# Kernel optimization log

Hardware: AMD Instinct MI355X
Metric: run time of the kernel (lower is better)

The kernel has to match this reference:

```python
import jax, jax.numpy as jnp
import numpy as np

B, IN_F, K_INT, OUT_F = 256, 512, 75, 64
INIT = 0.05


def setup_inputs() -> dict:
    key = jax.random.key(0)
    k_x, k_t = jax.random.split(key)
    x = jax.random.normal(k_x, (B, IN_F), dtype=jnp.float32)
    T = jax.random.normal(k_t, (IN_F, K_INT, OUT_F), dtype=jnp.float32) * INIT
    return {"x": x, "T": T}


def reference(x, T):
    # M: [B, K, O] = x @ T flattened over (K, O)
    Bn = x.shape[0]
    M = (x @ T.reshape(T.shape[0], -1)).reshape(Bn, T.shape[1], T.shape[2])
    # pairwise L1 distance over K: [B, B, O]
    # (original materializes [B, B, K, O] broadcasted diff; same math)
    M_diff = M[None, :, :, :] - M[:, None, :, :]
    distance = jnp.abs(M_diff).sum(axis=2)           # [B, B, O]
    exp_distance = jnp.exp(-distance)                # [B, B, O]
    minibatch_features = exp_distance.sum(axis=1) - 1.0  # [B, O]; -1 removes self-distance
    return minibatch_features
```

## Files before the change

### kernel.cpp

```cpp
#include <hip/hip_runtime.h>


typedef __attribute__((ext_vector_type(8))) short bf16x8;
typedef __attribute__((ext_vector_type(4))) float f32x4;
typedef unsigned short ushort_t;
typedef unsigned int uint_t;

__device__ inline ushort_t f2bf(float f) {
  uint_t u = __float_as_uint(f);
  return (ushort_t)((u + 0x7FFFu + ((u >> 16) & 1u)) >> 16);
}

__global__ __launch_bounds__(256) void cvt_x(const float* __restrict__ x,
                                             ushort_t* __restrict__ xb) {
  const int i = blockIdx.x * 256 + threadIdx.x;
  const float4* x4 = reinterpret_cast<const float4*>(x);
  const float4 v0 = x4[i * 2], v1 = x4[i * 2 + 1];
  uint4 o;
  o.x = (uint_t)f2bf(v0.x) | ((uint_t)f2bf(v0.y) << 16);
  o.y = (uint_t)f2bf(v0.z) | ((uint_t)f2bf(v0.w) << 16);
  o.z = (uint_t)f2bf(v1.x) | ((uint_t)f2bf(v1.y) << 16);
  o.w = (uint_t)f2bf(v1.z) | ((uint_t)f2bf(v1.w) << 16);
  *reinterpret_cast<uint4*>(xb + i * 8) = o;
}

__global__ __launch_bounds__(256) void cvt_T(const float* __restrict__ T,
                                             ushort_t* __restrict__ Tb) {
  const int f0 = blockIdx.x << 6;
  const int k = blockIdx.y;
  const int tid = threadIdx.x;
  __shared__ float tile[64][65];

  const float4* T4 = reinterpret_cast<const float4*>(T);
  const int r = tid >> 2;
  const int c = tid & 3;
#pragma unroll
  for (int h = 0; h < 4; ++h) {
    const int q = c + (h << 2);
    const float4 v = T4[(f0 + r) * 1200 + k * 16 + q];
    tile[r][(q << 2) + 0] = v.x;
    tile[r][(q << 2) + 1] = v.y;
    tile[r][(q << 2) + 2] = v.z;
    tile[r][(q << 2) + 3] = v.w;
  }
  __syncthreads();

  const int w = tid >> 2;
  ushort_t us[16];
#pragma unroll
  for (int j = 0; j < 16; ++j) us[j] = f2bf(tile[(c << 4) + j][w]);
  uint4 p0, p1;
  p0.x = (uint_t)us[0] | ((uint_t)us[1] << 16);
  p0.y = (uint_t)us[2] | ((uint_t)us[3] << 16);
  p0.z = (uint_t)us[4] | ((uint_t)us[5] << 16);
  p0.w = (uint_t)us[6] | ((uint_t)us[7] << 16);
  p1.x = (uint_t)us[8] | ((uint_t)us[9] << 16);
  p1.y = (uint_t)us[10] | ((uint_t)us[11] << 16);
  p1.z = (uint_t)us[12] | ((uint_t)us[13] << 16);
  p1.w = (uint_t)us[14] | ((uint_t)us[15] << 16);
  uint4* dst = reinterpret_cast<uint4*>(Tb + ((k << 6) + w) * 512 + f0 + (c << 4));
  dst[0] = p0;
  dst[1] = p1;
}

__global__ __launch_bounds__(256) void md_gemm_mfma(const ushort_t* __restrict__ Tb,
                                                    const ushort_t* __restrict__ xb,
                                                    float* __restrict__ Mt) {
  const int tid = threadIdx.x;
  const int l = tid & 63, w = tid >> 6;
  const int n0 = (blockIdx.x << 6) + ((w >> 1) << 5);
  const int b0 = (blockIdx.y << 6) + ((w & 1) << 5);
  const int lr = l & 15;
  const int ko = (l >> 4) << 3;

  const ushort_t* pa0 = Tb + (n0 + lr) * 512 + ko;
  const ushort_t* pa1 = pa0 + 16 * 512;
  const ushort_t* pb0 = xb + (b0 + lr) * 512 + ko;
  const ushort_t* pb1 = pb0 + 16 * 512;

  f32x4 d00 = {0.f, 0.f, 0.f, 0.f}, d01 = d00, d10 = d00, d11 = d00;

#pragma unroll 4
  for (int kk = 0; kk < 16; ++kk) {
    const int off = kk << 5;
    const bf16x8 a0 = *reinterpret_cast<const bf16x8*>(pa0 + off);
    const bf16x8 a1 = *reinterpret_cast<const bf16x8*>(pa1 + off);
    const bf16x8 f0 = *reinterpret_cast<const bf16x8*>(pb0 + off);
    const bf16x8 f1 = *reinterpret_cast<const bf16x8*>(pb1 + off);
    d00 = __builtin_amdgcn_mfma_f32_16x16x32_bf16(a0, f0, d00, 0, 0, 0);
    d01 = __builtin_amdgcn_mfma_f32_16x16x32_bf16(a0, f1, d01, 0, 0, 0);
    d10 = __builtin_amdgcn_mfma_f32_16x16x32_bf16(a1, f0, d10, 0, 0, 0);
    d11 = __builtin_amdgcn_mfma_f32_16x16x32_bf16(a1, f1, d11, 0, 0, 0);
  }

#pragma unroll
  for (int r = 0; r < 4; ++r) {
    const int row = ((l >> 4) << 2) + r;
    {
      const int n = n0 + row;
      float* base = Mt + (n & 63) * 19200 + (n >> 6) * 256;
      base[b0 + lr] = d00[r];
      base[b0 + 16 + lr] = d01[r];
    }
    {
      const int n = n0 + 16 + row;
      float* base = Mt + (n & 63) * 19200 + (n >> 6) * 256;
      base[b0 + lr] = d10[r];
      base[b0 + 16 + lr] = d11[r];
    }
  }
}

__global__ __launch_bounds__(256) void md_pair(const float* __restrict__ Mt,
                                               float* __restrict__ out) {
  const int o = blockIdx.x;
  const int ibase = blockIdx.y << 5;
  const int tid = threadIdx.x;
  const int io = tid & 15;
  const int jg = tid >> 4;

  __shared__ alignas(16) float Ms[38 * 256];

  float d0[16], d1[16];
#pragma unroll
  for (int q = 0; q < 16; ++q) { d0[q] = 0.0f; d1[q] = 0.0f; }

  const int i0 = ibase + (io << 1);

  for (int kh = 0; kh < 2; ++kh) {
    const int nk = kh ? 37 : 38;
    {
      const float4* src4 = reinterpret_cast<const float4*>(Mt + o * 19200 + kh * (38 * 256));
      float4* dst4 = reinterpret_cast<float4*>(Ms);
      const int n4 = nk << 6;
      for (int idx = tid; idx < n4; idx += 256) dst4[idx] = src4[idx];
    }
    __syncthreads();

    for (int k = 0; k < nk; ++k) {
      const float* row = Ms + (k << 8);
      const float mi0 = row[i0];
      const float mi1 = row[i0 + 1];
      const float4* row4 = reinterpret_cast<const float4*>(row) + (jg << 2);
#pragma unroll
      for (int q = 0; q < 4; ++q) {
        const float4 v = row4[q];
        d0[4 * q + 0] += __builtin_fabsf(v.x - mi0);
        d0[4 * q + 1] += __builtin_fabsf(v.y - mi0);
        d0[4 * q + 2] += __builtin_fabsf(v.z - mi0);
        d0[4 * q + 3] += __builtin_fabsf(v.w - mi0);
        d1[4 * q + 0] += __builtin_fabsf(v.x - mi1);
        d1[4 * q + 1] += __builtin_fabsf(v.y - mi1);
        d1[4 * q + 2] += __builtin_fabsf(v.z - mi1);
        d1[4 * q + 3] += __builtin_fabsf(v.w - mi1);
      }
    }
    __syncthreads();
  }

  float s0 = 0.0f, s1 = 0.0f;
#pragma unroll
  for (int q = 0; q < 16; ++q) {
    s0 += __expf(-d0[q]);
    s1 += __expf(-d1[q]);
  }

  float* red = Ms;
  red[((io << 1) + 0) * 17 + jg] = s0;
  red[((io << 1) + 1) * 17 + jg] = s1;
  __syncthreads();
  if (tid < 32) {
    float s = 0.0f;
#pragma unroll
    for (int g = 0; g < 16; ++g) s += red[tid * 17 + g];
    out[(ibase + tid) * 64 + o] = s - 1.0f;
  }
}

extern "C" void kernel_launch(void* const* d_in, const int* in_sizes, int n_in,
                              void* d_out, int out_size, void* d_ws, size_t ws_size,
                              hipStream_t stream) {
  const float* x = (const float*)d_in[0];
  const float* T = (const float*)d_in[1];
  float* out = (float*)d_out;

  char* ws = (char*)d_ws;
  float* Mt = (float*)ws;
  ushort_t* Tb = (ushort_t*)(ws + 4915200);
  ushort_t* xb = (ushort_t*)(ws + 9830400);

  cvt_x<<<64, 256, 0, stream>>>(x, xb);
  cvt_T<<<dim3(8, 75), 256, 0, stream>>>(T, Tb);
  md_gemm_mfma<<<dim3(75, 4), 256, 0, stream>>>(Tb, xb, Mt);
  md_pair<<<dim3(64, 8), 256, 0, stream>>>(Mt, out);
}
```

Measured before the change: 57.73 us.

## Fuse MFMA GEMM into pairwise L1 kernel, keeping M tile in LDS

Merges the GEMM and pairwise-distance kernels. Each block recomputes M[:, :, o] for all 256 batch rows with MFMA straight into shared memory, which removes the global Mt round trip and one launch. T is re-laid out padded to 80 K-rows per output feature, and the 37.5KB... wait, 80x276 floats (about 88KB) of LDS holds all 75 K rows at once, so the two-phase reload goes away. The cost is that each of the 4 i-blocks per o redoes the same GEMM, and the large LDS footprint with 512 threads limits occupancy.

After: 87.35 us. 1.51x slower.

```diff
diff --git a/kernel.cpp b/kernel.cpp
--- a/kernel.cpp
+++ b/kernel.cpp
@@ -3,40 +3,50 @@
 
 typedef __attribute__((ext_vector_type(8))) short bf16x8;
 typedef __attribute__((ext_vector_type(4))) float f32x4;
-typedef unsigned short ushort_t;
-typedef unsigned int uint_t;
+typedef unsigned short u16;
+typedef unsigned int u32;
 
-__device__ inline ushort_t f2bf(float f) {
-  uint_t u = __float_as_uint(f);
-  return (ushort_t)((u + 0x7FFFu + ((u >> 16) & 1u)) >> 16);
+__device__ inline u16 f2bf(float f) {
+  u32 u = __float_as_uint(f);
+  return (u16)((u + 0x7FFFu + ((u >> 16) & 1u)) >> 16);
 }
 
 __global__ __launch_bounds__(256) void cvt_x(const float* __restrict__ x,
-                                             ushort_t* __restrict__ xb) {
+                                             u16* __restrict__ xb) {
   const int i = blockIdx.x * 256 + threadIdx.x;
   const float4* x4 = reinterpret_cast<const float4*>(x);
   const float4 v0 = x4[i * 2], v1 = x4[i * 2 + 1];
   uint4 o;
-  o.x = (uint_t)f2bf(v0.x) | ((uint_t)f2bf(v0.y) << 16);
-  o.y = (uint_t)f2bf(v0.z) | ((uint_t)f2bf(v0.w) << 16);
-  o.z = (uint_t)f2bf(v1.x) | ((uint_t)f2bf(v1.y) << 16);
-  o.w = (uint_t)f2bf(v1.z) | ((uint_t)f2bf(v1.w) << 16);
+  o.x = (u32)f2bf(v0.x) | ((u32)f2bf(v0.y) << 16);
+  o.y = (u32)f2bf(v0.z) | ((u32)f2bf(v0.w) << 16);
+  o.z = (u32)f2bf(v1.x) | ((u32)f2bf(v1.y) << 16);
+  o.w = (u32)f2bf(v1.z) | ((u32)f2bf(v1.w) << 16);
   *reinterpret_cast<uint4*>(xb + i * 8) = o;
 }
 
 __global__ __launch_bounds__(256) void cvt_T(const float* __restrict__ T,
-                                             ushort_t* __restrict__ Tb) {
+                                             u16* __restrict__ Tb) {
   const int f0 = blockIdx.x << 6;
   const int k = blockIdx.y;
   const int tid = threadIdx.x;
+  const int w = tid >> 2;
+  const int c = tid & 3;
+  u16* dst = Tb + (w * 80 + k) * 512 + f0 + (c << 4);
+
+  if (k >= 75) {
+    const uint4 z = make_uint4(0, 0, 0, 0);
+    reinterpret_cast<uint4*>(dst)[0] = z;
+    reinterpret_cast<uint4*>(dst)[1] = z;
+    return;
+  }
+
   __shared__ float tile[64][65];
-
   const float4* T4 = reinterpret_cast<const float4*>(T);
-  const int r = tid >> 2;
-  const int c = tid & 3;
 #pragma unroll
   for (int h = 0; h < 4; ++h) {
-    const int q = c + (h << 2);
+    const int idx = (h << 8) + tid;
+    const int r = idx >> 4;
+    const int q = idx & 15;
     const float4 v = T4[(f0 + r) * 1200 + k * 16 + q];
     tile[r][(q << 2) + 0] = v.x;
     tile[r][(q << 2) + 1] = v.y;
@@ -45,131 +55,102 @@
   }
   __syncthreads();
 
-  const int w = tid >> 2;
-  ushort_t us[16];
+  u16 us[16];
 #pragma unroll
   for (int j = 0; j < 16; ++j) us[j] = f2bf(tile[(c << 4) + j][w]);
   uint4 p0, p1;
-  p0.x = (uint_t)us[0] | ((uint_t)us[1] << 16);
-  p0.y = (uint_t)us[2] | ((uint_t)us[3] << 16);
-  p0.z = (uint_t)us[4] | ((uint_t)us[5] << 16);
-  p0.w = (uint_t)us[6] | ((uint_t)us[7] << 16);
-  p1.x = (uint_t)us[8] | ((uint_t)us[9] << 16);
-  p1.y = (uint_t)us[10] | ((uint_t)us[11] << 16);
-  p1.z = (uint_t)us[12] | ((uint_t)us[13] << 16);
-  p1.w = (uint_t)us[14] | ((uint_t)us[15] << 16);
-  uint4* dst = reinterpret_cast<uint4*>(Tb + ((k << 6) + w) * 512 + f0 + (c << 4));
-  dst[0] = p0;
-  dst[1] = p1;
+  p0.x = (u32)us[0] | ((u32)us[1] << 16);
+  p0.y = (u32)us[2] | ((u32)us[3] << 16);
+  p0.z = (u32)us[4] | ((u32)us[5] << 16);
+  p0.w = (u32)us[6] | ((u32)us[7] << 16);
+  p1.x = (u32)us[8] | ((u32)us[9] << 16);
+  p1.y = (u32)us[10] | ((u32)us[11] << 16);
+  p1.z = (u32)us[12] | ((u32)us[13] << 16);
+  p1.w = (u32)us[14] | ((u32)us[15] << 16);
+  reinterpret_cast<uint4*>(dst)[0] = p0;
+  reinterpret_cast<uint4*>(dst)[1] = p1;
 }
 
-__global__ __launch_bounds__(256) void md_gemm_mfma(const ushort_t* __restrict__ Tb,
-                                                    const ushort_t* __restrict__ xb,
-                                                    float* __restrict__ Mt) {
+#define MROW 276
+__global__ __launch_bounds__(512, 2) void md_fused(const u16* __restrict__ Tb,
+                                                   const u16* __restrict__ xb,
+                                                   float* __restrict__ out) {
+  const int o = blockIdx.x;
+  const int ibase = blockIdx.y << 6;
   const int tid = threadIdx.x;
-  const int l = tid & 63, w = tid >> 6;
-  const int n0 = (blockIdx.x << 6) + ((w >> 1) << 5);
-  const int b0 = (blockIdx.y << 6) + ((w & 1) << 5);
-  const int lr = l & 15;
-  const int ko = (l >> 4) << 3;
 
-  const ushort_t* pa0 = Tb + (n0 + lr) * 512 + ko;
-  const ushort_t* pa1 = pa0 + 16 * 512;
-  const ushort_t* pb0 = xb + (b0 + lr) * 512 + ko;
-  const ushort_t* pb1 = pb0 + 16 * 512;
+  __shared__ float Ms[80 * MROW];
 
-  f32x4 d00 = {0.f, 0.f, 0.f, 0.f}, d01 = d00, d10 = d00, d11 = d00;
-
+  {
+    const int l = tid & 63, w = tid >> 6;
+    const int b0 = w << 5;
+    const int lr = l & 15;
+    const int ko = (l >> 4) << 3;
+    const u16* A = Tb + o * (80 * 512);
+    const u16* B0 = xb + (b0 + lr) * 512 + ko;
+    const u16* B1 = B0 + 16 * 512;
+#pragma unroll
+    for (int kt = 0; kt < 5; ++kt) {
+      const u16* Ak = A + (kt * 16 + lr) * 512 + ko;
+      f32x4 d0 = {0.f, 0.f, 0.f, 0.f}, d1 = d0;
 #pragma unroll 4
-  for (int kk = 0; kk < 16; ++kk) {
-    const int off = kk << 5;
-    const bf16x8 a0 = *reinterpret_cast<const bf16x8*>(pa0 + off);
-    const bf16x8 a1 = *reinterpret_cast<const bf16x8*>(pa1 + off);
-    const bf16x8 f0 = *reinterpret_cast<const bf16x8*>(pb0 + off);
-    const bf16x8 f1 = *reinterpret_cast<const bf16x8*>(pb1 + off);
-    d00 = __builtin_amdgcn_mfma_f32_16x16x32_bf16(a0, f0, d00, 0, 0, 0);
-    d01 = __builtin_amdgcn_mfma_f32_16x16x32_bf16(a0, f1, d01, 0, 0, 0);
-    d10 = __builtin_amdgcn_mfma_f32_16x16x32_bf16(a1, f0, d10, 0, 0, 0);
-    d11 = __builtin_amdgcn_mfma_f32_16x16x32_bf16(a1, f1, d11, 0, 0, 0);
-  }
-
+      for (int ks = 0; ks < 16; ++ks) {
+        const bf16x8 a  = *reinterpret_cast<const bf16x8*>(Ak + (ks << 5));
+        const bf16x8 f0 = *reinterpret_cast<const bf16x8*>(B0 + (ks << 5));
+        const bf16x8 f1 = *reinterpret_cast<const bf16x8*>(B1 + (ks << 5));
+        d0 = __builtin_amdgcn_mfma_f32_16x16x32_bf16(a, f0, d0, 0, 0, 0);
+        d1 = __builtin_amdgcn_mfma_f32_16x16x32_bf16(a, f1, d1, 0, 0, 0);
+      }
 #pragma unroll
-  for (int r = 0; r < 4; ++r) {
-    const int row = ((l >> 4) << 2) + r;
-    {
-      const int n = n0 + row;
-      float* base = Mt + (n & 63) * 19200 + (n >> 6) * 256;
-      base[b0 + lr] = d00[r];
-      base[b0 + 16 + lr] = d01[r];
-    }
-    {
-      const int n = n0 + 16 + row;
-      float* base = Mt + (n & 63) * 19200 + (n >> 6) * 256;
-      base[b0 + lr] = d10[r];
-      base[b0 + 16 + lr] = d11[r];
+      for (int r = 0; r < 4; ++r) {
+        const int k = kt * 16 + ((l >> 4) << 2) + r;
+        Ms[k * MROW + b0 + lr] = d0[r];
+        Ms[k * MROW + b0 + 16 + lr] = d1[r];
+      }
     }
   }
-}
+  __syncthreads();
 
-__global__ __launch_bounds__(256) void md_pair(const float* __restrict__ Mt,
-                                               float* __restrict__ out) {
-  const int o = blockIdx.x;
-  const int ibase = blockIdx.y << 5;
-  const int tid = threadIdx.x;
-  const int io = tid & 15;
-  const int jg = tid >> 4;
+  const int io = tid & 31;
+  const int jg = tid >> 5;
+  const int iL = ibase + (io << 1);
 
-  __shared__ alignas(16) float Ms[38 * 256];
+  float d0a[16], d1a[16];
+#pragma unroll
+  for (int q = 0; q < 16; ++q) { d0a[q] = 0.0f; d1a[q] = 0.0f; }
 
-  float d0[16], d1[16];
+  for (int k = 0; k < 75; ++k) {
+    const float* row = Ms + k * MROW;
+    const float mi0 = row[iL];
+    const float mi1 = row[iL + 1];
+    const float4* row4 = reinterpret_cast<const float4*>(row) + (jg << 2);
 #pragma unroll
-  for (int q = 0; q < 16; ++q) { d0[q] = 0.0f; d1[q] = 0.0f; }
-
-  const int i0 = ibase + (io << 1);
-
-  for (int kh = 0; kh < 2; ++kh) {
-    const int nk = kh ? 37 : 38;
-    {
-      const float4* src4 = reinterpret_cast<const float4*>(Mt + o * 19200 + kh * (38 * 256));
-      float4* dst4 = reinterpret_cast<float4*>(Ms);
-      const int n4 = nk << 6;
-      for (int idx = tid; idx < n4; idx += 256) dst4[idx] = src4[idx];
+    for (int q = 0; q < 4; ++q) {
+      const float4 v = row4[q];
+      d0a[4 * q + 0] += __builtin_fabsf(v.x - mi0);
+      d0a[4 * q + 1] += __builtin_fabsf(v.y - mi0);
+      d0a[4 * q + 2] += __builtin_fabsf(v.z - mi0);
+      d0a[4 * q + 3] += __builtin_fabsf(v.w - mi0);
+      d1a[4 * q + 0] += __builtin_fabsf(v.x - mi1);
+      d1a[4 * q + 1] += __builtin_fabsf(v.y - mi1);
+      d1a[4 * q + 2] += __builtin_fabsf(v.z - mi1);
+      d1a[4 * q + 3] += __builtin_fabsf(v.w - mi1);
     }
-    __syncthreads();
-
-    for (int k = 0; k < nk; ++k) {
-      const float* row = Ms + (k << 8);
-      const float mi0 = row[i0];
-      const float mi1 = row[i0 + 1];
-      const float4* row4 = reinterpret_cast<const float4*>(row) + (jg << 2);
-#pragma unroll
-      for (int q = 0; q < 4; ++q) {
-        const float4 v = row4[q];
-        d0[4 * q + 0] += __builtin_fabsf(v.x - mi0);
-        d0[4 * q + 1] += __builtin_fabsf(v.y - mi0);
-        d0[4 * q + 2] += __builtin_fabsf(v.z - mi0);
-        d0[4 * q + 3] += __builtin_fabsf(v.w - mi0);
-        d1[4 * q + 0] += __builtin_fabsf(v.x - mi1);
-        d1[4 * q + 1] += __builtin_fabsf(v.y - mi1);
-        d1[4 * q + 2] += __builtin_fabsf(v.z - mi1);
-        d1[4 * q + 3] += __builtin_fabsf(v.w - mi1);
-      }
-    }
-    __syncthreads();
   }
 
   float s0 = 0.0f, s1 = 0.0f;
 #pragma unroll
   for (int q = 0; q < 16; ++q) {
-    s0 += __expf(-d0[q]);
-    s1 += __expf(-d1[q]);
+    s0 += __expf(-d0a[q]);
+    s1 += __expf(-d1a[q]);
   }
 
+  __syncthreads();
   float* red = Ms;
   red[((io << 1) + 0) * 17 + jg] = s0;
   red[((io << 1) + 1) * 17 + jg] = s1;
   __syncthreads();
-  if (tid < 32) {
+  if (tid < 64) {
     float s = 0.0f;
 #pragma unroll
     for (int g = 0; g < 16; ++g) s += red[tid * 17 + g];
@@ -185,12 +166,10 @@
   float* out = (float*)d_out;
 
   char* ws = (char*)d_ws;
-  float* Mt = (float*)ws;
-  ushort_t* Tb = (ushort_t*)(ws + 4915200);
-  ushort_t* xb = (ushort_t*)(ws + 9830400);
+  u16* Tb = (u16*)ws;
+  u16* xb = (u16*)(ws + 5242880);
 
   cvt_x<<<64, 256, 0, stream>>>(x, xb);
-  cvt_T<<<dim3(8, 75), 256, 0, stream>>>(T, Tb);
-  md_gemm_mfma<<<dim3(75, 4), 256, 0, stream>>>(Tb, xb, Mt);
-  md_pair<<<dim3(64, 8), 256, 0, stream>>>(Mt, out);
+  cvt_T<<<dim3(8, 80), 256, 0, stream>>>(T, Tb);
+  md_fused<<<dim3(64, 4), 512, 0, stream>>>(Tb, xb, out);
 }
```

## Exploit distance symmetry with upper-triangular tile pairs and a reduce kernel

Applied to the files above, without the earlier changes.

The pairwise kernel now computes only the upper-triangular 64x64 tile pairs of the batch-by-batch distance matrix for each output feature. Each off-diagonal tile contributes both row sums and column sums to the partial results, and a new reduce kernel adds the partials and subtracts the self term. Each thread now computes a 4x4 register block from float4 loads instead of 2x16. This cuts the abs-diff arithmetic by roughly 40% but adds a kernel launch, extra reductions and more shared memory per block (about 38KB).

Measured after the change: 53.24 us. 1.08x faster.

```diff
diff --git a/kernel.cpp b/kernel.cpp
--- a/kernel.cpp
+++ b/kernel.cpp
@@ -3,29 +3,29 @@
 
 typedef __attribute__((ext_vector_type(8))) short bf16x8;
 typedef __attribute__((ext_vector_type(4))) float f32x4;
-typedef unsigned short ushort_t;
-typedef unsigned int uint_t;
-
-__device__ inline ushort_t f2bf(float f) {
-  uint_t u = __float_as_uint(f);
-  return (ushort_t)((u + 0x7FFFu + ((u >> 16) & 1u)) >> 16);
+typedef unsigned short u16;
+typedef unsigned int u32;
+
+__device__ inline u16 f2bf(float f) {
+  u32 u = __float_as_uint(f);
+  return (u16)((u + 0x7FFFu + ((u >> 16) & 1u)) >> 16);
 }
 
 __global__ __launch_bounds__(256) void cvt_x(const float* __restrict__ x,
-                                             ushort_t* __restrict__ xb) {
+                                             u16* __restrict__ xb) {
   const int i = blockIdx.x * 256 + threadIdx.x;
   const float4* x4 = reinterpret_cast<const float4*>(x);
   const float4 v0 = x4[i * 2], v1 = x4[i * 2 + 1];
   uint4 o;
-  o.x = (uint_t)f2bf(v0.x) | ((uint_t)f2bf(v0.y) << 16);
-  o.y = (uint_t)f2bf(v0.z) | ((uint_t)f2bf(v0.w) << 16);
-  o.z = (uint_t)f2bf(v1.x) | ((uint_t)f2bf(v1.y) << 16);
-  o.w = (uint_t)f2bf(v1.z) | ((uint_t)f2bf(v1.w) << 16);
+  o.x = (u32)f2bf(v0.x) | ((u32)f2bf(v0.y) << 16);
+  o.y = (u32)f2bf(v0.z) | ((u32)f2bf(v0.w) << 16);
+  o.z = (u32)f2bf(v1.x) | ((u32)f2bf(v1.y) << 16);
+  o.w = (u32)f2bf(v1.z) | ((u32)f2bf(v1.w) << 16);
   *reinterpret_cast<uint4*>(xb + i * 8) = o;
 }
 
 __global__ __launch_bounds__(256) void cvt_T(const float* __restrict__ T,
-                                             ushort_t* __restrict__ Tb) {
+                                             u16* __restrict__ Tb) {
   const int f0 = blockIdx.x << 6;
   const int k = blockIdx.y;
   const int tid = threadIdx.x;
@@ -46,25 +46,25 @@
   __syncthreads();
 
   const int w = tid >> 2;
-  ushort_t us[16];
+  u16 us[16];
 #pragma unroll
   for (int j = 0; j < 16; ++j) us[j] = f2bf(tile[(c << 4) + j][w]);
   uint4 p0, p1;
-  p0.x = (uint_t)us[0] | ((uint_t)us[1] << 16);
-  p0.y = (uint_t)us[2] | ((uint_t)us[3] << 16);
-  p0.z = (uint_t)us[4] | ((uint_t)us[5] << 16);
-  p0.w = (uint_t)us[6] | ((uint_t)us[7] << 16);
-  p1.x = (uint_t)us[8] | ((uint_t)us[9] << 16);
-  p1.y = (uint_t)us[10] | ((uint_t)us[11] << 16);
-  p1.z = (uint_t)us[12] | ((uint_t)us[13] << 16);
-  p1.w = (uint_t)us[14] | ((uint_t)us[15] << 16);
+  p0.x = (u32)us[0] | ((u32)us[1] << 16);
+  p0.y = (u32)us[2] | ((u32)us[3] << 16);
+  p0.z = (u32)us[4] | ((u32)us[5] << 16);
+  p0.w = (u32)us[6] | ((u32)us[7] << 16);
+  p1.x = (u32)us[8] | ((u32)us[9] << 16);
+  p1.y = (u32)us[10] | ((u32)us[11] << 16);
+  p1.z = (u32)us[12] | ((u32)us[13] << 16);
+  p1.w = (u32)us[14] | ((u32)us[15] << 16);
   uint4* dst = reinterpret_cast<uint4*>(Tb + ((k << 6) + w) * 512 + f0 + (c << 4));
   dst[0] = p0;
   dst[1] = p1;
 }
 
-__global__ __launch_bounds__(256) void md_gemm_mfma(const ushort_t* __restrict__ Tb,
-                                                    const ushort_t* __restrict__ xb,
+__global__ __launch_bounds__(256) void md_gemm_mfma(const u16* __restrict__ Tb,
+                                                    const u16* __restrict__ xb,
                                                     float* __restrict__ Mt) {
   const int tid = threadIdx.x;
   const int l = tid & 63, w = tid >> 6;
@@ -73,10 +73,10 @@
   const int lr = l & 15;
   const int ko = (l >> 4) << 3;
 
-  const ushort_t* pa0 = Tb + (n0 + lr) * 512 + ko;
-  const ushort_t* pa1 = pa0 + 16 * 512;
-  const ushort_t* pb0 = xb + (b0 + lr) * 512 + ko;
-  const ushort_t* pb1 = pb0 + 16 * 512;
+  const u16* pa0 = Tb + (n0 + lr) * 512 + ko;
+  const u16* pa1 = pa0 + 16 * 512;
+  const u16* pb0 = xb + (b0 + lr) * 512 + ko;
+  const u16* pb1 = pb0 + 16 * 512;
 
   f32x4 d00 = {0.f, 0.f, 0.f, 0.f}, d01 = d00, d10 = d00, d11 = d00;
 
@@ -111,70 +111,102 @@
   }
 }
 
-__global__ __launch_bounds__(256) void md_pair(const float* __restrict__ Mt,
-                                               float* __restrict__ out) {
-  const int o = blockIdx.x;
-  const int ibase = blockIdx.y << 5;
+__global__ __launch_bounds__(256) void md_pair_sym(const float* __restrict__ Mt,
+                                                   float* __restrict__ ps) {
+  const int bid = blockIdx.x;
+  const int o = bid & 63;
+  const int tp = bid >> 6;
+  const int TI[10] = {0, 0, 0, 0, 1, 1, 1, 2, 2, 3};
+  const int TJ[10] = {0, 1, 2, 3, 1, 2, 3, 2, 3, 3};
+  const int ti = TI[tp], tj = TJ[tp];
   const int tid = threadIdx.x;
+  const bool diag = (ti == tj);
+
+  __shared__ alignas(16) float sm[2 * 75 * 64];
+  float4* Mi4 = reinterpret_cast<float4*>(sm);
+  float4* Mj4 = diag ? Mi4 : Mi4 + 75 * 16;
+
+  {
+    const float4* src = reinterpret_cast<const float4*>(Mt + o * 19200 + ti * 64);
+    for (int t = tid; t < 1200; t += 256) {
+      const int k = t >> 4, q = t & 15;
+      Mi4[k * 16 + q] = src[k * 64 + q];
+    }
+    if (!diag) {
+      const float4* srj = reinterpret_cast<const float4*>(Mt + o * 19200 + tj * 64);
+      for (int t = tid; t < 1200; t += 256) {
+        const int k = t >> 4, q = t & 15;
+        Mj4[k * 16 + q] = srj[k * 64 + q];
+      }
+    }
+  }
+  __syncthreads();
+
   const int io = tid & 15;
-  const int jg = tid >> 4;
-
-  __shared__ alignas(16) float Ms[38 * 256];
-
-  float d0[16], d1[16];
-#pragma unroll
-  for (int q = 0; q < 16; ++q) { d0[q] = 0.0f; d1[q] = 0.0f; }
-
-  const int i0 = ibase + (io << 1);
-
-  for (int kh = 0; kh < 2; ++kh) {
-    const int nk = kh ? 37 : 38;
-    {
-      const float4* src4 = reinterpret_cast<const float4*>(Mt + o * 19200 + kh * (38 * 256));
-      float4* dst4 = reinterpret_cast<float4*>(Ms);
-      const int n4 = nk << 6;
-      for (int idx = tid; idx < n4; idx += 256) dst4[idx] = src4[idx];
-    }
+  const int js = tid >> 4;
+
+  float d[4][4];
+#pragma unroll
+  for (int a = 0; a < 4; ++a)
+#pragma unroll
+    for (int b = 0; b < 4; ++b) d[a][b] = 0.0f;
+
+  for (int k = 0; k < 75; ++k) {
+    const float4 vi = Mi4[k * 16 + io];
+    const float4 vj = Mj4[k * 16 + js];
+    const float via[4] = {vi.x, vi.y, vi.z, vi.w};
+    const float vja[4] = {vj.x, vj.y, vj.z, vj.w};
+#pragma unroll
+    for (int a = 0; a < 4; ++a)
+#pragma unroll
+      for (int b = 0; b < 4; ++b) d[a][b] += __builtin_fabsf(vja[b] - via[a]);
+  }
+
+  float isum[4] = {0.f, 0.f, 0.f, 0.f};
+  float jsum[4] = {0.f, 0.f, 0.f, 0.f};
+#pragma unroll
+  for (int a = 0; a < 4; ++a)
+#pragma unroll
+    for (int b = 0; b < 4; ++b) {
+      const float e = __expf(-d[a][b]);
+      isum[a] += e;
+      jsum[b] += e;
+    }
+
+  __syncthreads();
+  float* red = sm;
+#pragma unroll
+  for (int a = 0; a < 4; ++a) red[((io << 2) + a) * 17 + js] = isum[a];
+  __syncthreads();
+  if (tid < 64) {
+    float s = 0.0f;
+#pragma unroll
+    for (int c = 0; c < 16; ++c) s += red[tid * 17 + c];
+    ps[(((o << 2) + ti) << 2 | tj) * 64 + tid] = s;
+  }
+  if (!diag) {
     __syncthreads();
-
-    for (int k = 0; k < nk; ++k) {
-      const float* row = Ms + (k << 8);
-      const float mi0 = row[i0];
-      const float mi1 = row[i0 + 1];
-      const float4* row4 = reinterpret_cast<const float4*>(row) + (jg << 2);
-#pragma unroll
-      for (int q = 0; q < 4; ++q) {
-        const float4 v = row4[q];
-        d0[4 * q + 0] += __builtin_fabsf(v.x - mi0);
-        d0[4 * q + 1] += __builtin_fabsf(v.y - mi0);
-        d0[4 * q + 2] += __builtin_fabsf(v.z - mi0);
-        d0[4 * q + 3] += __builtin_fabsf(v.w - mi0);
-        d1[4 * q + 0] += __builtin_fabsf(v.x - mi1);
-        d1[4 * q + 1] += __builtin_fabsf(v.y - mi1);
-        d1[4 * q + 2] += __builtin_fabsf(v.z - mi1);
-        d1[4 * q + 3] += __builtin_fabsf(v.w - mi1);
-      }
-    }
+#pragma unroll
+    for (int b = 0; b < 4; ++b) red[((js << 2) + b) * 17 + io] = jsum[b];
     __syncthreads();
-  }
-
-  float s0 = 0.0f, s1 = 0.0f;
-#pragma unroll
-  for (int q = 0; q < 16; ++q) {
-    s0 += __expf(-d0[q]);
-    s1 += __expf(-d1[q]);
-  }
-
-  float* red = Ms;
-  red[((io << 1) + 0) * 17 + jg] = s0;
-  red[((io << 1) + 1) * 17 + jg] = s1;
-  __syncthreads();
-  if (tid < 32) {
-    float s = 0.0f;
-#pragma unroll
-    for (int g = 0; g < 16; ++g) s += red[tid * 17 + g];
-    out[(ibase + tid) * 64 + o] = s - 1.0f;
-  }
+    if (tid < 64) {
+      float s = 0.0f;
+#pragma unroll
+      for (int c = 0; c < 16; ++c) s += red[tid * 17 + c];
+      ps[(((o << 2) + tj) << 2 | ti) * 64 + tid] = s;
+    }
+  }
+}
+
+__global__ __launch_bounds__(256) void md_reduce(const float* __restrict__ ps,
+                                                 float* __restrict__ out) {
+  const int idx = blockIdx.x * 256 + threadIdx.x;
+  const int i = idx >> 6, o = idx & 63;
+  const int g = i >> 6, il = i & 63;
+  float s = 0.0f;
+#pragma unroll
+  for (int c = 0; c < 4; ++c) s += ps[(((o << 2) + g) << 2 | c) * 64 + il];
+  out[i * 64 + o] = s - 1.0f;
 }
 
 extern "C" void kernel_launch(void* const* d_in, const int* in_sizes, int n_in,
@@ -186,11 +218,13 @@
 
   char* ws = (char*)d_ws;
   float* Mt = (float*)ws;
-  ushort_t* Tb = (ushort_t*)(ws + 4915200);
-  ushort_t* xb = (ushort_t*)(ws + 9830400);
+  u16* Tb = (u16*)(ws + 4915200);
+  u16* xb = (u16*)(ws + 9830400);
+  float* ps = (float*)(ws + 10092544);
 
   cvt_x<<<64, 256, 0, stream>>>(x, xb);
   cvt_T<<<dim3(8, 75), 256, 0, stream>>>(T, Tb);
   md_gemm_mfma<<<dim3(75, 4), 256, 0, stream>>>(Tb, xb, Mt);
-  md_pair<<<dim3(64, 8), 256, 0, stream>>>(Mt, out);
-}
+  md_pair_sym<<<640, 256, 0, stream>>>(Mt, ps);
+  md_reduce<<<64, 256, 0, stream>>>(ps, out);
+}
```
